# Optimization experiments

Measured on AMD Instinct MI355X. Metric: run time of the kernel, lower is better.

## Reference

```python
import jax, jax.numpy as jnp
import numpy as np

C = 1536          # interim_dim
D2 = 2 * C        # 3072, fc_nlb dim
LN_EPS = 1e-5


def setup_inputs() -> dict:
    key = jax.random.key(0)
    ks = jax.random.split(key, 24)
    B, L = 32, 1024
    s = 0.02
    inp = {
        "x": jax.random.normal(ks[0], (B, C), dtype=jnp.float32),
        "lfb_feats": jax.random.normal(ks[1], (B, L, C), dtype=jnp.float32),
        # 1x1 Conv1d weights act as (C_out, C_in) matmuls
        "theta_w": jax.random.normal(ks[2], (C, C), dtype=jnp.float32) * s,
        "theta_b": jnp.zeros((C,), dtype=jnp.float32),
        "phi_w": jax.random.normal(ks[3], (C, C), dtype=jnp.float32) * s,
        "phi_b": jnp.zeros((C,), dtype=jnp.float32),
        "gi_w": jax.random.normal(ks[4], (C, C), dtype=jnp.float32) * s,
        "gi_b": jnp.zeros((C,), dtype=jnp.float32),
        "ln_g": jnp.ones((C,), dtype=jnp.float32),
        "ln_b": jnp.zeros((C,), dtype=jnp.float32),
        "fc_w": jax.random.normal(ks[5], (C, C), dtype=jnp.float32) * s,
        "fc_b": jnp.zeros((C,), dtype=jnp.float32),
        "fc_nlb_w": jax.random.normal(ks[6], (D2, D2), dtype=jnp.float32) * s,
        "fc_nlb_b": jnp.zeros((D2,), dtype=jnp.float32),
        "fc1_w": jax.random.normal(ks[7], (1, 1024), dtype=jnp.float32) * s,
        "fc1_b": jnp.zeros((1,), dtype=jnp.float32),
        "fc2_w": jax.random.normal(ks[8], (1, 1024), dtype=jnp.float32) * s,
        "fc2_b": jnp.zeros((1,), dtype=jnp.float32),
        "fc3_w": jax.random.normal(ks[9], (1, 1024), dtype=jnp.float32) * s,
        "fc3_b": jnp.zeros((1,), dtype=jnp.float32),
        "fct_w": jax.random.normal(ks[10], (1, D2), dtype=jnp.float32) * s,
        "fct_b": jnp.zeros((1,), dtype=jnp.float32),
    }
    return inp


def _layernorm(x, g, b):
    mu = jnp.mean(x, axis=-1, keepdims=True)
    var = jnp.mean(jnp.square(x - mu), axis=-1, keepdims=True)
    return (x - mu) * jax.lax.rsqrt(var + LN_EPS) * g + b


def reference(x, lfb_feats, theta_w, theta_b, phi_w, phi_b, gi_w, gi_b,
              ln_g, ln_b, fc_w, fc_b, fc_nlb_w, fc_nlb_b,
              fc1_w, fc1_b, fc2_w, fc2_b, fc3_w, fc3_b, fct_w, fct_b):
    # --- _NLBlock on feats = x.unsqueeze(1): query sequence length is 1 ---
    # note: scale = 1/sqrt(1/C) = sqrt(C) (as in the original code)
    scale = jnp.sqrt(jnp.asarray(C, dtype=x.dtype))
    theta = x @ theta_w.T + theta_b                       # (B, C)
    phi = lfb_feats @ phi_w.T + phi_b                     # (B, L, C)
    gi = lfb_feats @ gi_w.T + gi_b                        # (B, L, C)
    scores = jnp.einsum('bc,blc->bl', theta, phi) * scale  # (B, L)
    attn = jax.nn.softmax(scores, axis=-1)
    o = jnp.einsum('bl,blc->bc', attn, gi)                # (B, C)
    o = jax.nn.relu(_layernorm(o, ln_g, ln_b))
    o = o @ fc_w.T + fc_b                                 # dropout -> identity (eval)
    longterm = o + x                                      # residual, (B, C)

    # --- head ---
    feats = jnp.concatenate([x, longterm], axis=1)        # (B, 2C)
    feats = jax.nn.relu(feats @ fc_nlb_w.T + fc_nlb_b)    # dropout -> identity
    f1 = feats[:, :1024]
    f2 = feats[:, 1024:2048]
    f3 = feats[:, 2048:3072]
    p1 = f1 @ fc1_w.T + fc1_b
    p2 = f2 @ fc2_w.T + fc2_b
    p3 = f3 @ fc3_w.T + fc3_b
    pt = feats @ fct_w.T + fct_b
    return jnp.concatenate([p1, p2, p3, pt], axis=1)      # (B, 4)
```

## Files before the change

kernel.cpp:

```cpp
#include <hip/hip_runtime.h>
#include <math.h>

#define B 32
#define C 1536
#define D2 3072
#define L 1024
#define KC 64
#define CH 16
#define LPW 16

__device__ inline float dot4(float4 a, float4 b) {
    return a.x * b.x + a.y * b.y + a.z * b.z + a.w * b.w;
}
__device__ inline float4 ld4(const float* p) { return *(const float4*)p; }
__device__ inline void   st4(float* p, float4 v) { *(float4*)p = v; }

__device__ inline int sw(int row, int q) {
    return row * KC + ((q ^ ((row >> 2) & 7)) << 2);
}

__global__ __launch_bounds__(256) void transpose_k(const float* __restrict__ src,
                                                   float* __restrict__ dst, int n) {
    __shared__ float tile[32][33];
    int bx = blockIdx.x * 32, by = blockIdx.y * 32;
    int tx = threadIdx.x & 31, ty0 = threadIdx.x >> 5;
    #pragma unroll
    for (int r = 0; r < 4; ++r) {
        int ty = ty0 + r * 8;
        tile[ty][tx] = src[(size_t)(by + ty) * n + bx + tx];
    }
    __syncthreads();
    #pragma unroll
    for (int r = 0; r < 4; ++r) {
        int ty = ty0 + r * 8;
        dst[(size_t)(bx + ty) * n + by + tx] = tile[tx][ty];
    }
}

__global__ __launch_bounds__(256) void gemm32(const float* __restrict__ A,
                                              const float* __restrict__ W,
                                              float* __restrict__ part,
                                              int N, int K, int kchunks) {
    __shared__ float xs[32 * KC];
    __shared__ float wsm[64 * KC];
    int tid = threadIdx.x;
    int j0 = blockIdx.x * 64;
    int kb = blockIdx.y;
    int tb = tid & 15;
    int tj = tid >> 4;

    float4 acc0 = make_float4(0.f, 0.f, 0.f, 0.f);
    float4 acc1 = make_float4(0.f, 0.f, 0.f, 0.f);

    for (int c = 0; c < kchunks; ++c) {
        int k0 = (kb * kchunks + c) * KC;
        __syncthreads();
        #pragma unroll
        for (int p = 0; p < 2; ++p) {
            int f = tid + 256 * p;
            int row = f >> 4, q = f & 15;
            st4(xs + sw(row, q), ld4(A + (size_t)row * K + k0 + 4 * q));
        }
        #pragma unroll
        for (int p = 0; p < 4; ++p) {
            int f = tid + 256 * p;
            int row = f >> 4, q = f & 15;
            st4(wsm + sw(row, q), ld4(W + (size_t)(j0 + row) * K + k0 + 4 * q));
        }
        __syncthreads();
        #pragma unroll
        for (int kq = 0; kq < 16; ++kq) {
            float4 x0 = ld4(xs + sw(2 * tb, kq));
            float4 x1 = ld4(xs + sw(2 * tb + 1, kq));
            float4 w0 = ld4(wsm + sw(4 * tj + 0, kq));
            float4 w1 = ld4(wsm + sw(4 * tj + 1, kq));
            float4 w2 = ld4(wsm + sw(4 * tj + 2, kq));
            float4 w3 = ld4(wsm + sw(4 * tj + 3, kq));
            acc0.x += dot4(x0, w0); acc0.y += dot4(x0, w1);
            acc0.z += dot4(x0, w2); acc0.w += dot4(x0, w3);
            acc1.x += dot4(x1, w0); acc1.y += dot4(x1, w1);
            acc1.z += dot4(x1, w2); acc1.w += dot4(x1, w3);
        }
    }
    st4(part + ((size_t)kb * 32 + 2 * tb + 0) * N + j0 + 4 * tj, acc0);
    st4(part + ((size_t)kb * 32 + 2 * tb + 1) * N + j0 + 4 * tj, acc1);
}

__global__ __launch_bounds__(256) void reduce_part(const float* __restrict__ part,
                                                   const float* __restrict__ bias,
                                                   const float* __restrict__ addx,
                                                   float* __restrict__ out,
                                                   float* __restrict__ feats,
                                                   int N, int mode) {
    int i = blockIdx.x * 256 + threadIdx.x;
    int b = i / N, j = i % N;
    float s = 0.f;
    #pragma unroll
    for (int kk = 0; kk < 12; ++kk) s += part[((size_t)kk * 32 + b) * N + j];
    if (bias) s += bias[j];
    if (mode == 2) {
        float xv = addx[i];
        feats[(size_t)b * D2 + j] = xv;
        feats[(size_t)b * D2 + C + j] = s + xv;
    } else {
        out[i] = s;
    }
}

__global__ __launch_bounds__(256) void reduce_ln_relu(const float* __restrict__ part,
                                                      const float* __restrict__ bias,
                                                      const float* __restrict__ g,
                                                      const float* __restrict__ bt,
                                                      float* __restrict__ out) {
    int b = blockIdx.x, tid = threadIdx.x;
    __shared__ float r1[4], r2[4];
    float lv[6];
    float s1 = 0.f, s2 = 0.f;
    #pragma unroll
    for (int t = 0; t < 6; ++t) {
        int c = tid + 256 * t;
        float acc = 0.f;
        #pragma unroll
        for (int kk = 0; kk < 12; ++kk) acc += part[((size_t)kk * 32 + b) * C + c];
        acc += bias[c];
        lv[t] = acc; s1 += acc; s2 += acc * acc;
    }
    #pragma unroll
    for (int off = 32; off > 0; off >>= 1) {
        s1 += __shfl_xor(s1, off, 64);
        s2 += __shfl_xor(s2, off, 64);
    }
    int wave = tid >> 6, lane = tid & 63;
    if (lane == 0) { r1[wave] = s1; r2[wave] = s2; }
    __syncthreads();
    s1 = r1[0] + r1[1] + r1[2] + r1[3];
    s2 = r2[0] + r2[1] + r2[2] + r2[3];
    float mu = s1 / (float)C;
    float var = s2 / (float)C - mu * mu;
    float rstd = 1.0f / sqrtf(var + 1e-5f);
    #pragma unroll
    for (int t = 0; t < 6; ++t) {
        int c = tid + 256 * t;
        float y = (lv[t] - mu) * rstd * g[c] + bt[c];
        out[(size_t)b * C + c] = fmaxf(y, 0.f);
    }
}

__global__ __launch_bounds__(256) void flash_k(const float* __restrict__ u,
                                               const float* __restrict__ lfb,
                                               float* __restrict__ pm,
                                               float* __restrict__ ps,
                                               float* __restrict__ pv) {
    int chunk = blockIdx.x;
    int b = blockIdx.y;
    int wave = threadIdx.x >> 6;
    int lane = threadIdx.x & 63;
    int widx = chunk * 4 + wave;

    const float scale = 39.19183588453085f;

    float uu[24];
    const float* ub = u + (size_t)b * C;
    #pragma unroll
    for (int t = 0; t < 6; ++t)
        *(float4*)(uu + 4 * t) = ld4(ub + 4 * lane + 256 * t);

    float m = -INFINITY, s = 0.f;
    float vv[24];
    #pragma unroll
    for (int t = 0; t < 24; ++t) vv[t] = 0.f;

    int l0 = chunk * (L / CH) + wave;
    for (int i = 0; i < LPW; ++i) {
        int l = l0 + i * 4;
        const float* row = lfb + ((size_t)b * L + l) * C;
        float xx[24];
        #pragma unroll
        for (int t = 0; t < 6; ++t)
            *(float4*)(xx + 4 * t) = ld4(row + 4 * lane + 256 * t);
        float d = 0.f;
        #pragma unroll
        for (int t = 0; t < 24; ++t) d += xx[t] * uu[t];
        #pragma unroll
        for (int off = 32; off > 0; off >>= 1) d += __shfl_xor(d, off, 64);
        float score = d * scale;
        float mn = fmaxf(m, score);
        float alpha = __expf(m - mn);
        float p = __expf(score - mn);
        s = s * alpha + p;
        #pragma unroll
        for (int t = 0; t < 24; ++t) vv[t] = vv[t] * alpha + p * xx[t];
        m = mn;
    }

    if (lane == 0) { pm[b * 64 + widx] = m; ps[b * 64 + widx] = s; }
    float* pvb = pv + ((size_t)b * 64 + widx) * C;
    #pragma unroll
    for (int t = 0; t < 6; ++t)
        st4(pvb + 4 * lane + 256 * t, *(float4*)(vv + 4 * t));
}

__global__ __launch_bounds__(256) void combine_k(const float* __restrict__ pm,
                                                 const float* __restrict__ ps,
                                                 const float* __restrict__ pv,
                                                 float* __restrict__ v) {
    int cc = blockIdx.x;
    int b = blockIdx.y;
    int tid = threadIdx.x;
    __shared__ float coef[64];
    if (tid < 64) {
        float mj = pm[b * 64 + tid];
        float M = mj;
        #pragma unroll
        for (int off = 32; off > 0; off >>= 1) M = fmaxf(M, __shfl_xor(M, off, 64));
        float ej = expf(mj - M);
        float S = ps[b * 64 + tid] * ej;
        #pragma unroll
        for (int off = 32; off > 0; off >>= 1) S += __shfl_xor(S, off, 64);
        coef[tid] = ej / S;
    }
    __syncthreads();
    int c = cc * 256 + tid;
    float acc = 0.f;
    #pragma unroll 8
    for (int j = 0; j < 64; ++j)
        acc += coef[j] * pv[((size_t)b * 64 + j) * C + c];
    v[(size_t)b * C + c] = acc;
}

__global__ __launch_bounds__(256) void final_k(const float* __restrict__ partH,
                                               const float* __restrict__ fcn_b,
                                               const float* __restrict__ w1, const float* __restrict__ b1,
                                               const float* __restrict__ w2, const float* __restrict__ b2,
                                               const float* __restrict__ w3, const float* __restrict__ b3,
                                               const float* __restrict__ wt, const float* __restrict__ bt,
                                               float* __restrict__ out) {
    int b = blockIdx.x;
    int tid = threadIdx.x;
    float ph0 = 0.f, ph1 = 0.f, ph2 = 0.f, ptv = 0.f;
    #pragma unroll
    for (int t = 0; t < 12; ++t) {
        int j = tid + 256 * t;
        float s = 0.f;
        #pragma unroll
        for (int ss = 0; ss < 12; ++ss)
            s += partH[((size_t)ss * 32 + b) * D2 + j];
        s += fcn_b[j];
        s = fmaxf(s, 0.f);
        ptv += s * wt[j];
        int jj = tid + 256 * (t & 3);
        if (t < 4)       ph0 += s * w1[jj];
        else if (t < 8)  ph1 += s * w2[jj];
        else             ph2 += s * w3[jj];
    }
    #pragma unroll
    for (int off = 32; off > 0; off >>= 1) {
        ph0 += __shfl_xor(ph0, off, 64);
        ph1 += __shfl_xor(ph1, off, 64);
        ph2 += __shfl_xor(ph2, off, 64);
        ptv += __shfl_xor(ptv, off, 64);
    }
    __shared__ float red[4][4];
    int wave = tid >> 6, lane = tid & 63;
    if (lane == 0) {
        red[wave][0] = ph0; red[wave][1] = ph1; red[wave][2] = ph2; red[wave][3] = ptv;
    }
    __syncthreads();
    if (tid < 4) {
        float v = red[0][tid] + red[1][tid] + red[2][tid] + red[3][tid];
        float bias = (tid == 0) ? b1[0] : (tid == 1) ? b2[0] : (tid == 2) ? b3[0] : bt[0];
        out[b * 4 + tid] = v + bias;
    }
}

extern "C" void kernel_launch(void* const* d_in, const int* in_sizes, int n_in,
                              void* d_out, int out_size, void* d_ws, size_t ws_size,
                              hipStream_t stream) {
    (void)in_sizes; (void)n_in; (void)out_size; (void)ws_size;
    const float* x       = (const float*)d_in[0];
    const float* lfb     = (const float*)d_in[1];
    const float* theta_w = (const float*)d_in[2];
    const float* theta_b = (const float*)d_in[3];
    const float* phi_w   = (const float*)d_in[4];
    const float* gi_w    = (const float*)d_in[6];
    const float* gi_b    = (const float*)d_in[7];
    const float* ln_g    = (const float*)d_in[8];
    const float* ln_b    = (const float*)d_in[9];
    const float* fc_w    = (const float*)d_in[10];
    const float* fc_b    = (const float*)d_in[11];
    const float* fcn_w   = (const float*)d_in[12];
    const float* fcn_b   = (const float*)d_in[13];
    const float* w1 = (const float*)d_in[14]; const float* b1 = (const float*)d_in[15];
    const float* w2 = (const float*)d_in[16]; const float* b2 = (const float*)d_in[17];
    const float* w3 = (const float*)d_in[18]; const float* b3 = (const float*)d_in[19];
    const float* wt = (const float*)d_in[20]; const float* bt = (const float*)d_in[21];
    float* out = (float*)d_out;
    float* w = (float*)d_ws;

    float* phiT  = w;
    float* partT = w + 2359296;
    float* partU = w + 2949120;
    float* partG = w + 3538944;
    float* partF = w + 4128768;
    float* partH = w + 4718592;
    float* pv    = w + 5898240;
    float* pm    = w + 9043968;
    float* ps    = w + 9046016;
    float* theta = w + 9048064;
    float* u     = w + 9097216;
    float* vbuf  = w + 9146368;
    float* oln   = w + 9195520;
    float* feats = w + 9244672;

    transpose_k<<<dim3(48, 48), 256, 0, stream>>>(phi_w, phiT, C);

    gemm32<<<dim3(24, 12), 256, 0, stream>>>(x, theta_w, partT, C, C, 2);
    reduce_part<<<192, 256, 0, stream>>>(partT, theta_b, nullptr, theta, nullptr, C, 0);

    gemm32<<<dim3(24, 12), 256, 0, stream>>>(theta, phiT, partU, C, C, 2);
    reduce_part<<<192, 256, 0, stream>>>(partU, nullptr, nullptr, u, nullptr, C, 0);

    flash_k<<<dim3(CH, B), 256, 0, stream>>>(u, lfb, pm, ps, pv);
    combine_k<<<dim3(6, B), 256, 0, stream>>>(pm, ps, pv, vbuf);

    gemm32<<<dim3(24, 12), 256, 0, stream>>>(vbuf, gi_w, partG, C, C, 2);
    reduce_ln_relu<<<B, 256, 0, stream>>>(partG, gi_b, ln_g, ln_b, oln);

    gemm32<<<dim3(24, 12), 256, 0, stream>>>(oln, fc_w, partF, C, C, 2);
    reduce_part<<<192, 256, 0, stream>>>(partF, fc_b, x, nullptr, feats, C, 2);

    gemm32<<<dim3(48, 12), 256, 0, stream>>>(feats, fcn_w, partH, D2, D2, 4);

    final_k<<<B, 256, 0, stream>>>(partH, fcn_b, w1, b1, w2, b2, w3, b3, wt, bt, out);
}
```

Baseline: 440.3 us.

## Merge flash partials in-block and widen head GEMM tile to 128 columns

```diff
diff --git a/kernel.cpp b/kernel.cpp
--- a/kernel.cpp
+++ b/kernel.cpp
@@ -86,6 +86,60 @@
     st4(part + ((size_t)kb * 32 + 2 * tb + 1) * N + j0 + 4 * tj, acc1);
 }
 
+__global__ __launch_bounds__(256) void gemm32t4(const float* __restrict__ A,
+                                                const float* __restrict__ W,
+                                                float* __restrict__ part,
+                                                int N, int K, int kchunks) {
+    __shared__ float xs[32 * KC];
+    __shared__ float wsm[128 * KC];
+    int tid = threadIdx.x;
+    int j0 = blockIdx.x * 128;
+    int kb = blockIdx.y;
+    int tb = tid & 7;
+    int tj = tid >> 3;
+
+    float4 acc[4];
+    #pragma unroll
+    for (int r = 0; r < 4; ++r) acc[r] = make_float4(0.f, 0.f, 0.f, 0.f);
+
+    for (int c = 0; c < kchunks; ++c) {
+        int k0 = (kb * kchunks + c) * KC;
+        __syncthreads();
+        #pragma unroll
+        for (int p = 0; p < 2; ++p) {
+            int f = tid + 256 * p;
+            int row = f >> 4, q = f & 15;
+            st4(xs + sw(row, q), ld4(A + (size_t)row * K + k0 + 4 * q));
+        }
+        #pragma unroll
+        for (int p = 0; p < 8; ++p) {
+            int f = tid + 256 * p;
+            int row = f >> 4, q = f & 15;
+            st4(wsm + sw(row, q), ld4(W + (size_t)(j0 + row) * K + k0 + 4 * q));
+        }
+        __syncthreads();
+        #pragma unroll
+        for (int kq = 0; kq < 16; ++kq) {
+            float4 xq[4], wq[4];
+            #pragma unroll
+            for (int r = 0; r < 4; ++r) {
+                xq[r] = ld4(xs + sw(4 * tb + r, kq));
+                wq[r] = ld4(wsm + sw(4 * tj + r, kq));
+            }
+            #pragma unroll
+            for (int r = 0; r < 4; ++r) {
+                acc[r].x += dot4(xq[r], wq[0]);
+                acc[r].y += dot4(xq[r], wq[1]);
+                acc[r].z += dot4(xq[r], wq[2]);
+                acc[r].w += dot4(xq[r], wq[3]);
+            }
+        }
+    }
+    #pragma unroll
+    for (int r = 0; r < 4; ++r)
+        st4(part + ((size_t)kb * 32 + 4 * tb + r) * N + j0 + 4 * tj, acc[r]);
+}
+
 __global__ __launch_bounds__(256) void reduce_part(const float* __restrict__ part,
                                                    const float* __restrict__ bias,
                                                    const float* __restrict__ addx,
@@ -155,9 +209,12 @@
     int b = blockIdx.y;
     int wave = threadIdx.x >> 6;
     int lane = threadIdx.x & 63;
-    int widx = chunk * 4 + wave;
+    int tid = threadIdx.x;
 
     const float scale = 39.19183588453085f;
+
+    __shared__ float sm[4], ss[4];
+    __shared__ float vsh[4 * C];
 
     float uu[24];
     const float* ub = u + (size_t)b * C;
@@ -193,11 +250,34 @@
         m = mn;
     }
 
-    if (lane == 0) { pm[b * 64 + widx] = m; ps[b * 64 + widx] = s; }
-    float* pvb = pv + ((size_t)b * 64 + widx) * C;
-    #pragma unroll
-    for (int t = 0; t < 6; ++t)
-        st4(pvb + 4 * lane + 256 * t, *(float4*)(vv + 4 * t));
+    if (lane == 0) { sm[wave] = m; ss[wave] = s; }
+    __syncthreads();
+    float M = fmaxf(fmaxf(sm[0], sm[1]), fmaxf(sm[2], sm[3]));
+    float e = __expf(m - M);
+    #pragma unroll
+    for (int t = 0; t < 6; ++t) {
+        float4 q = *(float4*)(vv + 4 * t);
+        q.x *= e; q.y *= e; q.z *= e; q.w *= e;
+        st4(vsh + wave * C + 4 * lane + 256 * t, q);
+    }
+    __syncthreads();
+    float* pvb = pv + ((size_t)b * 16 + chunk) * C;
+    for (int idx = tid; idx < 384; idx += 256) {
+        float4 a0 = ld4(vsh + 0 * C + 4 * idx);
+        float4 a1 = ld4(vsh + 1 * C + 4 * idx);
+        float4 a2 = ld4(vsh + 2 * C + 4 * idx);
+        float4 a3 = ld4(vsh + 3 * C + 4 * idx);
+        st4(pvb + 4 * idx, make_float4(a0.x + a1.x + a2.x + a3.x,
+                                       a0.y + a1.y + a2.y + a3.y,
+                                       a0.z + a1.z + a2.z + a3.z,
+                                       a0.w + a1.w + a2.w + a3.w));
+    }
+    if (tid == 0) {
+        float S = ss[0] * __expf(sm[0] - M) + ss[1] * __expf(sm[1] - M)
+                + ss[2] * __expf(sm[2] - M) + ss[3] * __expf(sm[3] - M);
+        pm[b * 16 + chunk] = M;
+        ps[b * 16 + chunk] = S;
+    }
 }
 
 __global__ __launch_bounds__(256) void combine_k(const float* __restrict__ pm,
@@ -207,25 +287,20 @@
     int cc = blockIdx.x;
     int b = blockIdx.y;
     int tid = threadIdx.x;
-    __shared__ float coef[64];
-    if (tid < 64) {
-        float mj = pm[b * 64 + tid];
-        float M = mj;
-        #pragma unroll
-        for (int off = 32; off > 0; off >>= 1) M = fmaxf(M, __shfl_xor(M, off, 64));
-        float ej = expf(mj - M);
-        float S = ps[b * 64 + tid] * ej;
-        #pragma unroll
-        for (int off = 32; off > 0; off >>= 1) S += __shfl_xor(S, off, 64);
-        coef[tid] = ej / S;
-    }
-    __syncthreads();
+    float mj[16], ej[16];
+    float M = -INFINITY;
+    #pragma unroll
+    for (int i = 0; i < 16; ++i) { mj[i] = pm[b * 16 + i]; M = fmaxf(M, mj[i]); }
+    float S = 0.f;
+    #pragma unroll
+    for (int i = 0; i < 16; ++i) { ej[i] = __expf(mj[i] - M); S += ps[b * 16 + i] * ej[i]; }
+    float inv = 1.0f / S;
     int c = cc * 256 + tid;
     float acc = 0.f;
-    #pragma unroll 8
-    for (int j = 0; j < 64; ++j)
-        acc += coef[j] * pv[((size_t)b * 64 + j) * C + c];
-    v[(size_t)b * C + c] = acc;
+    #pragma unroll
+    for (int i = 0; i < 16; ++i)
+        acc += ej[i] * pv[((size_t)b * 16 + i) * C + c];
+    v[(size_t)b * C + c] = acc * inv;
 }
 
 __global__ __launch_bounds__(256) void final_k(const float* __restrict__ partH,
@@ -304,13 +379,13 @@
     float* partF = w + 4128768;
     float* partH = w + 4718592;
     float* pv    = w + 5898240;
-    float* pm    = w + 9043968;
-    float* ps    = w + 9046016;
-    float* theta = w + 9048064;
-    float* u     = w + 9097216;
-    float* vbuf  = w + 9146368;
-    float* oln   = w + 9195520;
-    float* feats = w + 9244672;
+    float* pm    = w + 6684672;
+    float* ps    = w + 6685184;
+    float* theta = w + 6685696;
+    float* u     = w + 6734848;
+    float* vbuf  = w + 6784000;
+    float* oln   = w + 6833152;
+    float* feats = w + 6882304;
 
     transpose_k<<<dim3(48, 48), 256, 0, stream>>>(phi_w, phiT, C);
 
@@ -329,7 +404,7 @@
     gemm32<<<dim3(24, 12), 256, 0, stream>>>(oln, fc_w, partF, C, C, 2);
     reduce_part<<<192, 256, 0, stream>>>(partF, fc_b, x, nullptr, feats, C, 2);
 
-    gemm32<<<dim3(48, 12), 256, 0, stream>>>(feats, fcn_w, partH, D2, D2, 4);
+    gemm32t4<<<dim3(24, 12), 256, 0, stream>>>(feats, fcn_w, partH, D2, D2, 4);
 
     final_k<<<B, 256, 0, stream>>>(partH, fcn_b, w1, b1, w2, b2, w3, b3, wt, bt, out);
 }
```

New measurement: 473.7 us. 1.08x slower.
